# Kernel optimization log

Measured on AMD Instinct MI355X. Metric: run time of the kernel, lower is better.

The kernel has to match this reference:

```python
import jax, jax.numpy as jnp
import numpy as np

B, T, I, H, K, U = 16, 256, 64, 128, 64, 256
NOISE_INIT = 0.1

def lecun_tanh(x):
    return 1.7159 * jnp.tanh(0.666 * x)

def setup_inputs() -> dict:
    key = jax.random.key(0)
    ks = jax.random.split(key, 16)
    s_in = 1.0 / np.sqrt(I + H)
    s_bb = 1.0 / np.sqrt(U)
    inp = {
        "x": jax.random.normal(ks[0], (B, T, I), dtype=jnp.float32),
        "timespans": jax.random.uniform(ks[1], (B, T), dtype=jnp.float32, minval=0.05, maxval=1.0),
        "noise_eps": jax.random.normal(ks[2], (T, B, K, H), dtype=jnp.float32),
        # backbone: Linear(I+H -> U)
        "Wb": jax.random.normal(ks[3], (I + H, U), dtype=jnp.float32) * s_in,
        "bb": jnp.zeros((U,), dtype=jnp.float32),
        # CfC heads: Linear(U -> H) each
        "W_ff1": jax.random.normal(ks[4], (U, H), dtype=jnp.float32) * s_bb,
        "b_ff1": jnp.zeros((H,), dtype=jnp.float32),
        "W_ff2": jax.random.normal(ks[5], (U, H), dtype=jnp.float32) * s_bb,
        "b_ff2": jnp.zeros((H,), dtype=jnp.float32),
        "W_ta": jax.random.normal(ks[6], (U, H), dtype=jnp.float32) * s_bb,
        "b_ta": jnp.zeros((H,), dtype=jnp.float32),
        "W_tb": jax.random.normal(ks[7], (U, H), dtype=jnp.float32) * s_bb,
        "b_tb": jnp.zeros((H,), dtype=jnp.float32),
        # learnable time-scaled noise scale (per hidden unit)
        "noise_scale": jnp.full((H,), NOISE_INIT, dtype=jnp.float32),
    }
    return inp


def reference(x, timespans, noise_eps, Wb, bb, W_ff1, b_ff1, W_ff2, b_ff2,
              W_ta, b_ta, W_tb, b_tb, noise_scale):
    # initial particle state: zeros, uniform log-weights
    particles0 = jnp.zeros((B, K, H), dtype=x.dtype)
    log_w0 = jnp.full((B, K), -jnp.log(jnp.asarray(K, x.dtype)), dtype=x.dtype)

    def step(carry, inputs):
        particles, log_w = carry
        x_t, ts_t, eps_t = inputs  # [B,I], [B], [B,K,H]
        ts = ts_t[:, None, None]                                  # [B,1,1]
        xk = jnp.broadcast_to(x_t[:, None, :], (B, K, I))
        z = jnp.concatenate([xk, particles], axis=-1)             # [B,K,I+H]
        bbk = lecun_tanh(jnp.einsum('bku,uv->bkv', z, Wb) + bb)   # backbone [B,K,U]
        ff1 = jnp.tanh(jnp.einsum('bku,uh->bkh', bbk, W_ff1) + b_ff1)
        ff2 = jnp.tanh(jnp.einsum('bku,uh->bkh', bbk, W_ff2) + b_ff2)
        t_a = jnp.einsum('bku,uh->bkh', bbk, W_ta) + b_ta
        t_b = jnp.einsum('bku,uh->bkh', bbk, W_tb) + b_tb
        t_interp = jax.nn.sigmoid(t_a * ts + t_b)                 # CfC gate
        new_p = ff1 * (1.0 - t_interp) + t_interp * ff2           # [B,K,H]
        # time-scaled state noise injection
        new_p = new_p + noise_scale * jnp.sqrt(ts) * eps_t
        # weights stay uniform (no observations) -> ESS = K, no resampling
        w = jax.nn.softmax(log_w, axis=-1)                        # [B,K]
        out = jnp.einsum('bk,bkh->bh', w, new_p)                  # weighted mean
        return (new_p, log_w), out

    x_t = jnp.transpose(x, (1, 0, 2))        # [T,B,I]
    ts_t = jnp.transpose(timespans, (1, 0))  # [T,B]
    (particles, log_w), outs = jax.lax.scan(step, (particles0, log_w0),
                                            (x_t, ts_t, noise_eps))
    outputs = jnp.transpose(outs, (1, 0, 2))  # [B,T,H]
    return outputs, particles, log_w
```

## Files before the change

kernel.cpp:

```cpp
#include <hip/hip_runtime.h>
#include <math.h>

typedef __attribute__((ext_vector_type(8))) short short8;
typedef __attribute__((ext_vector_type(4))) float f32x4;

#define B_ 16
#define T_ 256
#define I_ 64
#define H_ 128
#define K_ 64
#define U_ 256
#define KC 16
#define NTHR 512

#define OUT_OFF_P (B_*T_*H_)
#define OUT_OFF_LW (OUT_OFF_P + B_*K_*H_)

__device__ __forceinline__ unsigned short f2bf(float x) {
    unsigned int u = __float_as_uint(x);
    u += 0x7fffu + ((u >> 16) & 1u);
    return (unsigned short)(u >> 16);
}
__device__ __forceinline__ float bf2f(unsigned short u) {
    return __uint_as_float(((unsigned int)u) << 16);
}
__device__ __forceinline__ float fast_tanh(float x) {
    float e = __expf(2.0f * x);
    return 1.0f - 2.0f * __builtin_amdgcn_rcpf(e + 1.0f);
}
__device__ __forceinline__ float fast_sigmoid(float x) {
    return __builtin_amdgcn_rcpf(1.0f + __expf(-x));
}
__device__ __forceinline__ unsigned int swzbyte_p(unsigned int row, unsigned int col) {
    return (row * 256u + col * 2u) ^ ((row & 7u) << 4);
}
__device__ __forceinline__ unsigned int swzbyte_b(unsigned int row, unsigned int pos) {
    return (row * 512u + pos * 2u) ^ ((row & 7u) << 4);
}

#define BAR() do { asm volatile("s_waitcnt lgkmcnt(0)" ::: "memory"); \
                   __builtin_amdgcn_s_barrier(); \
                   asm volatile("" ::: "memory"); } while (0)

#define MFMA16(a, bfrag, c) __builtin_amdgcn_mfma_f32_16x16x32_bf16((a), (bfrag), (c), 0, 0, 0)

__global__ __launch_bounds__(256) void xw_kernel(
    const float* __restrict__ x, const float* __restrict__ Wb,
    const float* __restrict__ bb, unsigned short* __restrict__ xw)
{
    const int tid  = threadIdx.x;
    const int lane = tid & 63;
    const int wv   = tid >> 6;
    const int ln15 = lane & 15;
    const int l4   = lane >> 4;
    const int bid  = blockIdx.x;
    const int b    = bid >> 4;
    const int t0   = (bid & 15) * 16;

    short8 Bx[2][4];
    float bbc[4];
    #pragma unroll
    for (int kt = 0; kt < 2; ++kt) {
        #pragma unroll
        for (int ct = 0; ct < 4; ++ct) {
            short8 f;
            const int col = wv * 64 + ct * 16 + ln15;
            #pragma unroll
            for (int j = 0; j < 8; ++j)
                f[j] = (short)f2bf(Wb[(kt * 32 + l4 * 8 + j) * U_ + col]);
            Bx[kt][ct] = f;
        }
    }
    #pragma unroll
    for (int ct = 0; ct < 4; ++ct) bbc[ct] = bb[wv * 64 + ct * 16 + ln15];

    short8 ax[2];
    #pragma unroll
    for (int kt = 0; kt < 2; ++kt) {
        const float* xp = &x[(size_t)(b * T_ + t0 + ln15) * I_ + kt * 32 + l4 * 8];
        short8 f;
        #pragma unroll
        for (int j = 0; j < 8; ++j) f[j] = (short)f2bf(xp[j]);
        ax[kt] = f;
    }
    const f32x4 z4 = {0.f, 0.f, 0.f, 0.f};
    f32x4 acc[4] = {z4, z4, z4, z4};
    #pragma unroll
    for (int kt = 0; kt < 2; ++kt) {
        #pragma unroll
        for (int ct = 0; ct < 4; ++ct) acc[ct] = MFMA16(ax[kt], Bx[kt][ct], acc[ct]);
    }
    #pragma unroll
    for (int ct = 0; ct < 4; ++ct) {
        #pragma unroll
        for (int r = 0; r < 4; ++r) {
            const int trow = t0 + l4 * 4 + r;
            xw[(size_t)(b * T_ + trow) * U_ + wv * 64 + ct * 16 + ln15] = f2bf(acc[ct][r] + bbc[ct]);
        }
    }
}

__global__ __launch_bounds__(NTHR, 2) void pf_kernel(
    const unsigned short* __restrict__ xw, const float* __restrict__ tspan,
    const float* __restrict__ eps, const float* __restrict__ Wb,
    const float* __restrict__ Wf1, const float* __restrict__ bf1,
    const float* __restrict__ Wf2, const float* __restrict__ bf2,
    const float* __restrict__ Wta, const float* __restrict__ bta,
    const float* __restrict__ Wtb, const float* __restrict__ btb,
    const float* __restrict__ nscale, float* __restrict__ out)
{
    const int tid  = threadIdx.x;
    const int lane = tid & 63;
    const int wv   = tid >> 6;
    const int ln15 = lane & 15;
    const int l4   = lane >> 4;
    const int bid  = blockIdx.x;
    const int b    = bid >> 2;
    const int k0   = (bid & 3) * KC;

    __shared__ unsigned short p_bf[KC * H_];
    __shared__ unsigned short bbk_bf[KC * U_];
    __shared__ float ts_lds[T_];

    for (int i = tid; i < KC * H_; i += NTHR) p_bf[i] = 0;
    for (int i = tid; i < T_; i += NTHR) ts_lds[i] = tspan[b * T_ + i];

    short8 B1p[4][2];
    #pragma unroll
    for (int kt = 0; kt < 4; ++kt) {
        #pragma unroll
        for (int ct = 0; ct < 2; ++ct) {
            short8 f;
            const int col = wv * 32 + ct * 16 + ln15;
            #pragma unroll
            for (int j = 0; j < 8; ++j)
                f[j] = (short)f2bf(Wb[(I_ + kt * 32 + l4 * 8 + j) * U_ + col]);
            B1p[kt][ct] = f;
        }
    }
    const float* Whp[4] = {Wf1, Wf2, Wta, Wtb};
    const int hc = wv * 16 + ln15;
    short8 B2[4][8];
    #pragma unroll
    for (int hd = 0; hd < 4; ++hd) {
        #pragma unroll
        for (int kt = 0; kt < 8; ++kt) {
            short8 f;
            #pragma unroll
            for (int j = 0; j < 8; ++j) {
                const int pos = l4 * 8 + j;
                const int kg  = kt * 32 + (pos >> 1) + ((pos & 1) << 4);
                f[j] = (short)f2bf(Whp[hd][kg * H_ + hc]);
            }
            B2[hd][kt] = f;
        }
    }
    const float bf1c = bf1[hc], bf2c = bf2[hc];
    const float btac = bta[hc], btbc = btb[hc];
    const float nscc = nscale[hc];

    if ((bid & 3) == 0 && tid < K_)
        out[OUT_OFF_LW + b * K_ + tid] = -4.1588830833596715f;

    __syncthreads();

    const float* ep0 = eps + ((size_t)(b * K_ + k0 + l4 * 4)) * H_ + hc;
    const unsigned short* xwp = xw + (size_t)b * T_ * U_ + wv * 32 + ln15;
    float ecur[4];
    #pragma unroll
    for (int r = 0; r < 4; ++r) ecur[r] = ep0[r * H_];
    float xw0c = bf2f(xwp[0]), xw1c = bf2f(xwp[16]);
    float tscur = ts_lds[0];

    const f32x4 zero4 = {0.f, 0.f, 0.f, 0.f};

    for (int t = 0; t < T_; ++t) {
        const int tn = (t + 1 < T_) ? t + 1 : t;
        const float* epn = ep0 + (size_t)tn * (B_ * K_ * H_);
        float enext[4];
        #pragma unroll
        for (int r = 0; r < 4; ++r) enext[r] = epn[r * H_];
        const float xw0n = bf2f(xwp[tn * U_]), xw1n = bf2f(xwp[tn * U_ + 16]);
        const float tsn = ts_lds[tn];

        f32x4 acc0 = {xw0c, xw0c, xw0c, xw0c};
        f32x4 acc1 = {xw1c, xw1c, xw1c, xw1c};
        #pragma unroll
        for (int kt = 0; kt < 4; ++kt) {
            const short8 ap = *(const short8*)((const char*)p_bf + swzbyte_p(ln15, kt * 32 + l4 * 8));
            acc0 = MFMA16(ap, B1p[kt][0], acc0);
            acc1 = MFMA16(ap, B1p[kt][1], acc1);
        }
        #pragma unroll
        for (int r = 0; r < 4; ++r) {
            const int row = l4 * 4 + r;
            const unsigned int q0 = f2bf(1.7159f * fast_tanh(0.666f * acc0[r]));
            const unsigned int q1 = f2bf(1.7159f * fast_tanh(0.666f * acc1[r]));
            *(unsigned int*)((char*)bbk_bf + swzbyte_b(row, wv * 32 + 2 * ln15)) = q0 | (q1 << 16);
        }
        BAR();

        f32x4 a_f1 = zero4, a_f2 = zero4, a_ta = zero4, a_tb = zero4;
        #pragma unroll
        for (int kt = 0; kt < 8; ++kt) {
            const short8 a = *(const short8*)((const char*)bbk_bf + swzbyte_b(ln15, kt * 32 + l4 * 8));
            a_f1 = MFMA16(a, B2[0][kt], a_f1);
            a_f2 = MFMA16(a, B2[1][kt], a_f2);
            a_ta = MFMA16(a, B2[2][kt], a_ta);
            a_tb = MFMA16(a, B2[3][kt], a_tb);
        }
        const float sq = sqrtf(tscur);
        float psum = 0.f;
        const bool last = (t == T_ - 1);
        #pragma unroll
        for (int r = 0; r < 4; ++r) {
            const int row = l4 * 4 + r;
            const float f1v = fast_tanh(a_f1[r] + bf1c);
            const float f2v = fast_tanh(a_f2[r] + bf2c);
            const float tiv = fast_sigmoid((a_ta[r] + btac) * tscur + (a_tb[r] + btbc));
            const float np  = f1v + tiv * (f2v - f1v) + nscc * sq * ecur[r];
            *(unsigned short*)((char*)p_bf + swzbyte_p(row, hc)) = f2bf(np);
            psum += np;
            if (last)
                out[OUT_OFF_P + (size_t)(b * K_ + k0 + row) * H_ + hc] = np;
        }
        psum += __shfl_xor(psum, 16);
        psum += __shfl_xor(psum, 32);
        if (lane < 16)
            atomicAdd(&out[(size_t)(b * T_ + t) * H_ + wv * 16 + lane], psum * (1.0f / 64.0f));

        #pragma unroll
        for (int r = 0; r < 4; ++r) ecur[r] = enext[r];
        xw0c = xw0n; xw1c = xw1n;
        tscur = tsn;
        BAR();
    }
}

extern "C" void kernel_launch(void* const* d_in, const int* in_sizes, int n_in,
                              void* d_out, int out_size, void* d_ws, size_t ws_size,
                              hipStream_t stream) {
    const float* x    = (const float*)d_in[0];
    const float* tsp  = (const float*)d_in[1];
    const float* eps  = (const float*)d_in[2];
    const float* Wb   = (const float*)d_in[3];
    const float* bb   = (const float*)d_in[4];
    const float* Wf1  = (const float*)d_in[5];
    const float* bf1  = (const float*)d_in[6];
    const float* Wf2  = (const float*)d_in[7];
    const float* bf2  = (const float*)d_in[8];
    const float* Wta  = (const float*)d_in[9];
    const float* bta  = (const float*)d_in[10];
    const float* Wtb  = (const float*)d_in[11];
    const float* btb  = (const float*)d_in[12];
    const float* nsc  = (const float*)d_in[13];
    float* out = (float*)d_out;
    unsigned short* xw = (unsigned short*)d_ws;

    (void)hipMemsetAsync(d_out, 0, (size_t)OUT_OFF_P * sizeof(float), stream);
    xw_kernel<<<dim3(256), dim3(256), 0, stream>>>(x, Wb, bb, xw);
    pf_kernel<<<dim3(64), dim3(NTHR), 0, stream>>>(
        xw, tsp, eps, Wb, Wf1, bf1, Wf2, bf2, Wta, bta, Wtb, btb, nsc, out);
}
```

Measured before the change: 493.9 us.

## Split backbone into two halves to overlap second half with head MFMAs

Backbone columns are reassigned so each wave computes one 16-column slice in each half of U. The first half is published to LDS, then the second half's MFMAs and tanh are overlapped with the head GEMM over the first half's K range, followed by an extra barrier. This shortens the dependent chain per timestep by interleaving work. The cost is an additional block barrier per step and narrower 16-bit LDS stores.

Result: slower. 565.1 us (+14.4%).

```diff
diff --git a/kernel.cpp b/kernel.cpp
--- a/kernel.cpp
+++ b/kernel.cpp
@@ -34,8 +34,8 @@
 __device__ __forceinline__ unsigned int swzbyte_p(unsigned int row, unsigned int col) {
     return (row * 256u + col * 2u) ^ ((row & 7u) << 4);
 }
-__device__ __forceinline__ unsigned int swzbyte_b(unsigned int row, unsigned int pos) {
-    return (row * 512u + pos * 2u) ^ ((row & 7u) << 4);
+__device__ __forceinline__ unsigned int swzbyte_b(unsigned int row, unsigned int col) {
+    return (row * 512u + col * 2u) ^ ((row & 7u) << 4);
 }
 
 #define BAR() do { asm volatile("s_waitcnt lgkmcnt(0)" ::: "memory"); \
@@ -131,7 +131,7 @@
         #pragma unroll
         for (int ct = 0; ct < 2; ++ct) {
             short8 f;
-            const int col = wv * 32 + ct * 16 + ln15;
+            const int col = ct * 128 + wv * 16 + ln15;
             #pragma unroll
             for (int j = 0; j < 8; ++j)
                 f[j] = (short)f2bf(Wb[(I_ + kt * 32 + l4 * 8 + j) * U_ + col]);
@@ -147,11 +147,8 @@
         for (int kt = 0; kt < 8; ++kt) {
             short8 f;
             #pragma unroll
-            for (int j = 0; j < 8; ++j) {
-                const int pos = l4 * 8 + j;
-                const int kg  = kt * 32 + (pos >> 1) + ((pos & 1) << 4);
-                f[j] = (short)f2bf(Whp[hd][kg * H_ + hc]);
-            }
+            for (int j = 0; j < 8; ++j)
+                f[j] = (short)f2bf(Whp[hd][(kt * 32 + l4 * 8 + j) * H_ + hc]);
             B2[hd][kt] = f;
         }
     }
@@ -165,11 +162,11 @@
     __syncthreads();
 
     const float* ep0 = eps + ((size_t)(b * K_ + k0 + l4 * 4)) * H_ + hc;
-    const unsigned short* xwp = xw + (size_t)b * T_ * U_ + wv * 32 + ln15;
+    const unsigned short* xwp = xw + (size_t)b * T_ * U_ + wv * 16 + ln15;
     float ecur[4];
     #pragma unroll
     for (int r = 0; r < 4; ++r) ecur[r] = ep0[r * H_];
-    float xw0c = bf2f(xwp[0]), xw1c = bf2f(xwp[16]);
+    float xw0c = bf2f(xwp[0]), xw1c = bf2f(xwp[128]);
     float tscur = ts_lds[0];
 
     const f32x4 zero4 = {0.f, 0.f, 0.f, 0.f};
@@ -180,29 +177,49 @@
         float enext[4];
         #pragma unroll
         for (int r = 0; r < 4; ++r) enext[r] = epn[r * H_];
-        const float xw0n = bf2f(xwp[tn * U_]), xw1n = bf2f(xwp[tn * U_ + 16]);
+        const float xw0n = bf2f(xwp[tn * U_]), xw1n = bf2f(xwp[tn * U_ + 128]);
         const float tsn = ts_lds[tn];
 
+        short8 ap[4];
+        #pragma unroll
+        for (int kt = 0; kt < 4; ++kt)
+            ap[kt] = *(const short8*)((const char*)p_bf + swzbyte_p(ln15, kt * 32 + l4 * 8));
         f32x4 acc0 = {xw0c, xw0c, xw0c, xw0c};
-        f32x4 acc1 = {xw1c, xw1c, xw1c, xw1c};
-        #pragma unroll
-        for (int kt = 0; kt < 4; ++kt) {
-            const short8 ap = *(const short8*)((const char*)p_bf + swzbyte_p(ln15, kt * 32 + l4 * 8));
-            acc0 = MFMA16(ap, B1p[kt][0], acc0);
-            acc1 = MFMA16(ap, B1p[kt][1], acc1);
-        }
+        #pragma unroll
+        for (int kt = 0; kt < 4; ++kt) acc0 = MFMA16(ap[kt], B1p[kt][0], acc0);
         #pragma unroll
         for (int r = 0; r < 4; ++r) {
             const int row = l4 * 4 + r;
-            const unsigned int q0 = f2bf(1.7159f * fast_tanh(0.666f * acc0[r]));
-            const unsigned int q1 = f2bf(1.7159f * fast_tanh(0.666f * acc1[r]));
-            *(unsigned int*)((char*)bbk_bf + swzbyte_b(row, wv * 32 + 2 * ln15)) = q0 | (q1 << 16);
+            *(unsigned short*)((char*)bbk_bf + swzbyte_b(row, wv * 16 + ln15)) =
+                f2bf(1.7159f * fast_tanh(0.666f * acc0[r]));
         }
         BAR();
 
         f32x4 a_f1 = zero4, a_f2 = zero4, a_ta = zero4, a_tb = zero4;
-        #pragma unroll
-        for (int kt = 0; kt < 8; ++kt) {
+        {
+            f32x4 acc1 = {xw1c, xw1c, xw1c, xw1c};
+            #pragma unroll
+            for (int kt = 0; kt < 4; ++kt) acc1 = MFMA16(ap[kt], B1p[kt][1], acc1);
+
+            #pragma unroll
+            for (int kt = 0; kt < 4; ++kt) {
+                const short8 a = *(const short8*)((const char*)bbk_bf + swzbyte_b(ln15, kt * 32 + l4 * 8));
+                a_f1 = MFMA16(a, B2[0][kt], a_f1);
+                a_f2 = MFMA16(a, B2[1][kt], a_f2);
+                a_ta = MFMA16(a, B2[2][kt], a_ta);
+                a_tb = MFMA16(a, B2[3][kt], a_tb);
+            }
+            #pragma unroll
+            for (int r = 0; r < 4; ++r) {
+                const int row = l4 * 4 + r;
+                *(unsigned short*)((char*)bbk_bf + swzbyte_b(row, 128 + wv * 16 + ln15)) =
+                    f2bf(1.7159f * fast_tanh(0.666f * acc1[r]));
+            }
+        }
+        BAR();
+
+        #pragma unroll
+        for (int kt = 4; kt < 8; ++kt) {
             const short8 a = *(const short8*)((const char*)bbk_bf + swzbyte_b(ln15, kt * 32 + l4 * 8));
             a_f1 = MFMA16(a, B2[0][kt], a_f1);
             a_f2 = MFMA16(a, B2[1][kt], a_f2);
```

## Halve block to 4 waves, each wave computing twice the output columns

Applied to the files above, without the earlier changes.

The per-block thread count drops from 512 to 256, so each wave now covers 64 backbone columns and 32 hidden columns. Per-wave register-resident weight fragments double, and launch bounds change to one block per CU. The aim is to cut barrier cost and wave-coordination overhead in the sequential time loop. In exchange it raises register pressure and leaves fewer waves to hide MFMA and memory latency.

Measured after the change: 769.4 us. +55.8%, slower.

```diff
diff --git a/kernel.cpp b/kernel.cpp
--- a/kernel.cpp
+++ b/kernel.cpp
@@ -11,7 +11,7 @@
 #define K_ 64
 #define U_ 256
 #define KC 16
-#define NTHR 512
+#define NTHR 256
 
 #define OUT_OFF_P (B_*T_*H_)
 #define OUT_OFF_LW (OUT_OFF_P + B_*K_*H_)
@@ -100,7 +100,7 @@
     }
 }
 
-__global__ __launch_bounds__(NTHR, 2) void pf_kernel(
+__global__ __launch_bounds__(NTHR, 1) void pf_kernel(
     const unsigned short* __restrict__ xw, const float* __restrict__ tspan,
     const float* __restrict__ eps, const float* __restrict__ Wb,
     const float* __restrict__ Wf1, const float* __restrict__ bf1,
@@ -125,13 +125,13 @@
     for (int i = tid; i < KC * H_; i += NTHR) p_bf[i] = 0;
     for (int i = tid; i < T_; i += NTHR) ts_lds[i] = tspan[b * T_ + i];
 
-    short8 B1p[4][2];
+    short8 B1p[4][4];
     #pragma unroll
     for (int kt = 0; kt < 4; ++kt) {
         #pragma unroll
-        for (int ct = 0; ct < 2; ++ct) {
+        for (int ct = 0; ct < 4; ++ct) {
             short8 f;
-            const int col = wv * 32 + ct * 16 + ln15;
+            const int col = wv * 64 + ct * 16 + ln15;
             #pragma unroll
             for (int j = 0; j < 8; ++j)
                 f[j] = (short)f2bf(Wb[(I_ + kt * 32 + l4 * 8 + j) * U_ + col]);
@@ -139,37 +139,49 @@
         }
     }
     const float* Whp[4] = {Wf1, Wf2, Wta, Wtb};
-    const int hc = wv * 16 + ln15;
-    short8 B2[4][8];
+    short8 B2[4][8][2];
     #pragma unroll
     for (int hd = 0; hd < 4; ++hd) {
         #pragma unroll
         for (int kt = 0; kt < 8; ++kt) {
-            short8 f;
-            #pragma unroll
-            for (int j = 0; j < 8; ++j) {
-                const int pos = l4 * 8 + j;
-                const int kg  = kt * 32 + (pos >> 1) + ((pos & 1) << 4);
-                f[j] = (short)f2bf(Whp[hd][kg * H_ + hc]);
+            #pragma unroll
+            for (int c2 = 0; c2 < 2; ++c2) {
+                short8 f;
+                const int hc2 = wv * 32 + c2 * 16 + ln15;
+                #pragma unroll
+                for (int j = 0; j < 8; ++j) {
+                    const int pos = l4 * 8 + j;
+                    const int kg  = kt * 32 + (pos >> 1) + ((pos & 1) << 4);
+                    f[j] = (short)f2bf(Whp[hd][kg * H_ + hc2]);
+                }
+                B2[hd][kt][c2] = f;
             }
-            B2[hd][kt] = f;
-        }
-    }
-    const float bf1c = bf1[hc], bf2c = bf2[hc];
-    const float btac = bta[hc], btbc = btb[hc];
-    const float nscc = nscale[hc];
+        }
+    }
+    float bf1c[2], bf2c[2], btac[2], btbc[2], nscc[2];
+    #pragma unroll
+    for (int c2 = 0; c2 < 2; ++c2) {
+        const int hc2 = wv * 32 + c2 * 16 + ln15;
+        bf1c[c2] = bf1[hc2]; bf2c[c2] = bf2[hc2];
+        btac[c2] = bta[hc2]; btbc[c2] = btb[hc2];
+        nscc[c2] = nscale[hc2];
+    }
 
     if ((bid & 3) == 0 && tid < K_)
         out[OUT_OFF_LW + b * K_ + tid] = -4.1588830833596715f;
 
     __syncthreads();
 
-    const float* ep0 = eps + ((size_t)(b * K_ + k0 + l4 * 4)) * H_ + hc;
-    const unsigned short* xwp = xw + (size_t)b * T_ * U_ + wv * 32 + ln15;
-    float ecur[4];
-    #pragma unroll
-    for (int r = 0; r < 4; ++r) ecur[r] = ep0[r * H_];
-    float xw0c = bf2f(xwp[0]), xw1c = bf2f(xwp[16]);
+    const float* ep0 = eps + ((size_t)(b * K_ + k0 + l4 * 4)) * H_ + wv * 32 + ln15;
+    const unsigned short* xwp = xw + (size_t)b * T_ * U_ + wv * 64 + ln15;
+    float ecur[2][4];
+    #pragma unroll
+    for (int c2 = 0; c2 < 2; ++c2)
+        #pragma unroll
+        for (int r = 0; r < 4; ++r) ecur[c2][r] = ep0[c2 * 16 + r * H_];
+    float xwc[4];
+    #pragma unroll
+    for (int ct = 0; ct < 4; ++ct) xwc[ct] = bf2f(xwp[ct * 16]);
     float tscur = ts_lds[0];
 
     const f32x4 zero4 = {0.f, 0.f, 0.f, 0.f};
@@ -177,61 +189,84 @@
     for (int t = 0; t < T_; ++t) {
         const int tn = (t + 1 < T_) ? t + 1 : t;
         const float* epn = ep0 + (size_t)tn * (B_ * K_ * H_);
-        float enext[4];
-        #pragma unroll
-        for (int r = 0; r < 4; ++r) enext[r] = epn[r * H_];
-        const float xw0n = bf2f(xwp[tn * U_]), xw1n = bf2f(xwp[tn * U_ + 16]);
+        float enext[2][4];
+        #pragma unroll
+        for (int c2 = 0; c2 < 2; ++c2)
+            #pragma unroll
+            for (int r = 0; r < 4; ++r) enext[c2][r] = epn[c2 * 16 + r * H_];
+        float xwn[4];
+        #pragma unroll
+        for (int ct = 0; ct < 4; ++ct) xwn[ct] = bf2f(xwp[tn * U_ + ct * 16]);
         const float tsn = ts_lds[tn];
 
-        f32x4 acc0 = {xw0c, xw0c, xw0c, xw0c};
-        f32x4 acc1 = {xw1c, xw1c, xw1c, xw1c};
+        f32x4 acc[4];
+        #pragma unroll
+        for (int ct = 0; ct < 4; ++ct) { f32x4 v = {xwc[ct], xwc[ct], xwc[ct], xwc[ct]}; acc[ct] = v; }
         #pragma unroll
         for (int kt = 0; kt < 4; ++kt) {
             const short8 ap = *(const short8*)((const char*)p_bf + swzbyte_p(ln15, kt * 32 + l4 * 8));
-            acc0 = MFMA16(ap, B1p[kt][0], acc0);
-            acc1 = MFMA16(ap, B1p[kt][1], acc1);
+            #pragma unroll
+            for (int ct = 0; ct < 4; ++ct) acc[ct] = MFMA16(ap, B1p[kt][ct], acc[ct]);
         }
         #pragma unroll
         for (int r = 0; r < 4; ++r) {
             const int row = l4 * 4 + r;
-            const unsigned int q0 = f2bf(1.7159f * fast_tanh(0.666f * acc0[r]));
-            const unsigned int q1 = f2bf(1.7159f * fast_tanh(0.666f * acc1[r]));
-            *(unsigned int*)((char*)bbk_bf + swzbyte_b(row, wv * 32 + 2 * ln15)) = q0 | (q1 << 16);
+            const unsigned int q0 = f2bf(1.7159f * fast_tanh(0.666f * acc[0][r]));
+            const unsigned int q1 = f2bf(1.7159f * fast_tanh(0.666f * acc[1][r]));
+            const unsigned int q2 = f2bf(1.7159f * fast_tanh(0.666f * acc[2][r]));
+            const unsigned int q3 = f2bf(1.7159f * fast_tanh(0.666f * acc[3][r]));
+            *(unsigned int*)((char*)bbk_bf + swzbyte_b(row, wv * 64 + 2 * ln15))      = q0 | (q1 << 16);
+            *(unsigned int*)((char*)bbk_bf + swzbyte_b(row, wv * 64 + 32 + 2 * ln15)) = q2 | (q3 << 16);
         }
         BAR();
 
-        f32x4 a_f1 = zero4, a_f2 = zero4, a_ta = zero4, a_tb = zero4;
+        f32x4 af1[2] = {zero4, zero4}, af2[2] = {zero4, zero4};
+        f32x4 ata[2] = {zero4, zero4}, atb[2] = {zero4, zero4};
         #pragma unroll
         for (int kt = 0; kt < 8; ++kt) {
             const short8 a = *(const short8*)((const char*)bbk_bf + swzbyte_b(ln15, kt * 32 + l4 * 8));
-            a_f1 = MFMA16(a, B2[0][kt], a_f1);
-            a_f2 = MFMA16(a, B2[1][kt], a_f2);
-            a_ta = MFMA16(a, B2[2][kt], a_ta);
-            a_tb = MFMA16(a, B2[3][kt], a_tb);
+            #pragma unroll
+            for (int c2 = 0; c2 < 2; ++c2) {
+                af1[c2] = MFMA16(a, B2[0][kt][c2], af1[c2]);
+                af2[c2] = MFMA16(a, B2[1][kt][c2], af2[c2]);
+                ata[c2] = MFMA16(a, B2[2][kt][c2], ata[c2]);
+                atb[c2] = MFMA16(a, B2[3][kt][c2], atb[c2]);
+            }
         }
         const float sq = sqrtf(tscur);
-        float psum = 0.f;
+        float ps[2] = {0.f, 0.f};
         const bool last = (t == T_ - 1);
         #pragma unroll
-        for (int r = 0; r < 4; ++r) {
-            const int row = l4 * 4 + r;
-            const float f1v = fast_tanh(a_f1[r] + bf1c);
-            const float f2v = fast_tanh(a_f2[r] + bf2c);
-            const float tiv = fast_sigmoid((a_ta[r] + btac) * tscur + (a_tb[r] + btbc));
-            const float np  = f1v + tiv * (f2v - f1v) + nscc * sq * ecur[r];
-            *(unsigned short*)((char*)p_bf + swzbyte_p(row, hc)) = f2bf(np);
-            psum += np;
-            if (last)
-                out[OUT_OFF_P + (size_t)(b * K_ + k0 + row) * H_ + hc] = np;
-        }
-        psum += __shfl_xor(psum, 16);
-        psum += __shfl_xor(psum, 32);
-        if (lane < 16)
-            atomicAdd(&out[(size_t)(b * T_ + t) * H_ + wv * 16 + lane], psum * (1.0f / 64.0f));
-
-        #pragma unroll
-        for (int r = 0; r < 4; ++r) ecur[r] = enext[r];
-        xw0c = xw0n; xw1c = xw1n;
+        for (int c2 = 0; c2 < 2; ++c2) {
+            const int hc2 = wv * 32 + c2 * 16 + ln15;
+            #pragma unroll
+            for (int r = 0; r < 4; ++r) {
+                const int row = l4 * 4 + r;
+                const float f1v = fast_tanh(af1[c2][r] + bf1c[c2]);
+                const float f2v = fast_tanh(af2[c2][r] + bf2c[c2]);
+                const float tiv = fast_sigmoid((ata[c2][r] + btac[c2]) * tscur + (atb[c2][r] + btbc[c2]));
+                const float np  = f1v + tiv * (f2v - f1v) + nscc[c2] * sq * ecur[c2][r];
+                *(unsigned short*)((char*)p_bf + swzbyte_p(row, hc2)) = f2bf(np);
+                ps[c2] += np;
+                if (last)
+                    out[OUT_OFF_P + (size_t)(b * K_ + k0 + row) * H_ + hc2] = np;
+            }
+        }
+        #pragma unroll
+        for (int c2 = 0; c2 < 2; ++c2) {
+            float p2 = ps[c2];
+            p2 += __shfl_xor(p2, 16);
+            p2 += __shfl_xor(p2, 32);
+            if (lane < 16)
+                atomicAdd(&out[(size_t)(b * T_ + t) * H_ + wv * 32 + c2 * 16 + lane], p2 * (1.0f / 64.0f));
+        }
+
+        #pragma unroll
+        for (int c2 = 0; c2 < 2; ++c2)
+            #pragma unroll
+            for (int r = 0; r < 4; ++r) ecur[c2][r] = enext[c2][r];
+        #pragma unroll
+        for (int ct = 0; ct < 4; ++ct) xwc[ct] = xwn[ct];
         tscur = tsn;
         BAR();
     }
```
